# Kernel optimization log

Measured on AMD Instinct MI355X. Metric: run time of the kernel, lower is better.

## Reference

```python
import jax, jax.numpy as jnp
import numpy as np

NB_POOLS = 256


def setup_inputs() -> dict:
    key = jax.random.key(0)
    x = jax.random.normal(key, (32, 32, 32, 512), dtype=jnp.float32)
    return {"x": x}


def reference(x) -> jnp.ndarray:
    B, R, C, F = x.shape
    nb_maps = R * C
    x3 = x.reshape(B, nb_maps, F)
    # self-correlation: (B, nb_maps, nb_maps), normalized by feature count
    corr = jnp.einsum('bmf,bnf->bmn', x3, x3) / F
    corr = corr.reshape(B, R, C, nb_maps)
    # percentile ranks into the descending-sorted correlation values
    ranks = jnp.round(jnp.linspace(1.0, nb_maps - 1, NB_POOLS)).astype(jnp.int32)
    # full descending sort along last axis (matches tf.nn.top_k k=nb_maps)
    x_sort = -jnp.sort(-corr, axis=-1)
    x_pool = x_sort[..., ranks]  # (B, R, C, NB_POOLS)
    return x_pool
```

## Files before the change

### kernel.cpp

```cpp
#include <hip/hip_runtime.h>


#define NMAPS 1024
#define FDIM 512
#define TM 16
#define NT 256

typedef __attribute__((ext_vector_type(8))) short short8_t;
typedef __attribute__((ext_vector_type(4))) float f32x4;
typedef _Float16 h2 __attribute__((ext_vector_type(2)));

#define SELD 0x03020504u
#define SELA 0x07060100u

__device__ __forceinline__ h2 h2min(h2 a, h2 b) { return __builtin_elementwise_min(a, b); }
__device__ __forceinline__ h2 h2max(h2 a, h2 b) { return __builtin_elementwise_max(a, b); }

__device__ __forceinline__ unsigned h2u(h2 x) { union { h2 h; unsigned u; } t; t.h = x; return t.u; }
__device__ __forceinline__ h2 u2h(unsigned x) { union { h2 h; unsigned u; } t; t.u = x; return t.h; }

__device__ __forceinline__ h2 h2swap(h2 v) {
  unsigned u = h2u(v);
  return u2h((u >> 16) | (u << 16));
}

__device__ __forceinline__ h2 h2shfl_xor(h2 v, int m) {
  union { h2 h; int i; } u;
  u.h = v;
  u.i = __shfl_xor(u.i, m, 64);
  return u.h;
}

__device__ __forceinline__ void ce_pair(h2& a, h2& b, bool d) {
  h2 mn = h2min(a, b), mx = h2max(a, b);
  a = d ? mx : mn;
  b = d ? mn : mx;
}

__device__ __forceinline__ h2 ce1(h2 w, unsigned sel) {
  h2 s = h2swap(w);
  h2 mn = h2min(w, s), mx = h2max(w, s);
#if __has_builtin(__builtin_amdgcn_perm)
  return u2h(__builtin_amdgcn_perm(h2u(mx), h2u(mn), sel));
#else
  h2 rd; rd[0] = mx[0]; rd[1] = mn[1];
  h2 ra; ra[0] = mn[0]; ra[1] = mx[1];
  return (sel == SELD) ? rd : ra;
#endif
}

__device__ __forceinline__ void intra_merge16(h2 w[8], bool d, unsigned sel) {
  ce_pair(w[0], w[4], d); ce_pair(w[1], w[5], d); ce_pair(w[2], w[6], d); ce_pair(w[3], w[7], d);
  ce_pair(w[0], w[2], d); ce_pair(w[1], w[3], d); ce_pair(w[4], w[6], d); ce_pair(w[5], w[7], d);
  ce_pair(w[0], w[1], d); ce_pair(w[2], w[3], d); ce_pair(w[4], w[5], d); ce_pair(w[6], w[7], d);
#pragma unroll
  for (int u = 0; u < 8; ++u) w[u] = ce1(w[u], sel);
}

__device__ __forceinline__ void sort16(h2 w[8], bool d, unsigned sd, unsigned si) {
  w[0] = ce1(w[0], sd); w[1] = ce1(w[1], si); w[2] = ce1(w[2], sd); w[3] = ce1(w[3], si);
  w[4] = ce1(w[4], sd); w[5] = ce1(w[5], si); w[6] = ce1(w[6], sd); w[7] = ce1(w[7], si);
  ce_pair(w[0], w[1], d); ce_pair(w[2], w[3], !d); ce_pair(w[4], w[5], d); ce_pair(w[6], w[7], !d);
  w[0] = ce1(w[0], sd); w[1] = ce1(w[1], sd); w[2] = ce1(w[2], si); w[3] = ce1(w[3], si);
  w[4] = ce1(w[4], sd); w[5] = ce1(w[5], sd); w[6] = ce1(w[6], si); w[7] = ce1(w[7], si);
  ce_pair(w[0], w[2], d); ce_pair(w[1], w[3], d); ce_pair(w[4], w[6], !d); ce_pair(w[5], w[7], !d);
  ce_pair(w[0], w[1], d); ce_pair(w[2], w[3], d); ce_pair(w[4], w[5], !d); ce_pair(w[6], w[7], !d);
  w[0] = ce1(w[0], sd); w[1] = ce1(w[1], sd); w[2] = ce1(w[2], sd); w[3] = ce1(w[3], sd);
  w[4] = ce1(w[4], si); w[5] = ce1(w[5], si); w[6] = ce1(w[6], si); w[7] = ce1(w[7], si);
  intra_merge16(w, d, sd);
}

__device__ __forceinline__ void cross_ce(h2 w[8], int m, bool keepmax) {
#pragma unroll
  for (int u = 0; u < 8; ++u) {
    h2 p = h2shfl_xor(w[u], m);
    h2 mn = h2min(w[u], p), mx = h2max(w[u], p);
    w[u] = keepmax ? mx : mn;
  }
}

template<int K>
__device__ __forceinline__ void bitonic_stage(h2 w8[8], int lane) {
  const bool laneDesc = (K >= 16) ? ((lane & (K >> 4)) == 0) : true;
#pragma unroll
  for (int j = 512; j >= 16; j >>= 1) {
    if (j > (K >> 1)) continue;
    const int m = j >> 4;
    const bool keepmax = (((lane & m) == 0) == laneDesc);
#pragma unroll
    for (int u = 0; u < 8; ++u) {
      h2 p = h2shfl_xor(w8[u], m);
      h2 mn = h2min(w8[u], p), mx = h2max(w8[u], p);
      w8[u] = keepmax ? mx : mn;
    }
  }
#pragma unroll
  for (int j = 8; j >= 2; j >>= 1) {
    if (j > (K >> 1)) continue;
    const int jw = j >> 1;
#pragma unroll
    for (int u = 0; u < 8; ++u) {
      if ((u & jw) == 0) {
        const int v = u | jw;
        const bool desc = (K <= 8) ? (((2 * u) & K) == 0) : laneDesc;
        h2 mn = h2min(w8[u], w8[v]), mx = h2max(w8[u], w8[v]);
        w8[u] = desc ? mx : mn;
        w8[v] = desc ? mn : mx;
      }
    }
  }
#pragma unroll
  for (int u = 0; u < 8; ++u) {
    const bool desc = (K <= 8) ? (((2 * u) & K) == 0) : laneDesc;
    h2 s = h2swap(w8[u]);
    h2 mn = h2min(w8[u], s), mx = h2max(w8[u], s);
    h2 rd = (h2){mx[0], mn[1]};
    h2 ra = (h2){mn[0], mx[1]};
    w8[u] = desc ? rd : ra;
  }
}

template<int K>
__device__ __forceinline__ void bitonic_stage_tail(h2 w8[8], int lane) {
  const bool laneDesc = ((lane & (K >> 4)) == 0);
#pragma unroll
  for (int j = 512; j >= 16; j >>= 1) {
    if (j > (K >> 1)) continue;
    const int m = j >> 4;
    cross_ce(w8, m, ((lane & m) == 0) == laneDesc);
  }
  intra_merge16(w8, laneDesc, laneDesc ? SELD : SELA);
}

__device__ __forceinline__ void run_bitonic(h2 w8[8], int lane) {
  bitonic_stage<2>(w8, lane);
  bitonic_stage<4>(w8, lane);
  bitonic_stage<8>(w8, lane);
  bitonic_stage<16>(w8, lane);
  bitonic_stage<32>(w8, lane);
  bitonic_stage<64>(w8, lane);
  bitonic_stage<128>(w8, lane);
  bitonic_stage<256>(w8, lane);
  bitonic_stage<512>(w8, lane);
  bitonic_stage<1024>(w8, lane);
}

__global__ __launch_bounds__(256) void cvt_bf16_kernel(const float* __restrict__ x,
                                                       short* __restrict__ xw, int n8) {
  int i = blockIdx.x * 256 + threadIdx.x;
  if (i >= n8) return;
  const float4* x4 = reinterpret_cast<const float4*>(x);
  float4 a = x4[i * 2], c = x4[i * 2 + 1];
  float f[8] = {a.x, a.y, a.z, a.w, c.x, c.y, c.z, c.w};
  union { short8_t v; short s[8]; } o;
#pragma unroll
  for (int j = 0; j < 8; ++j) {
    unsigned u = __float_as_uint(f[j]);
    u += 0x7fffu + ((u >> 16) & 1u);
    o.s[j] = (short)(u >> 16);
  }
  reinterpret_cast<short8_t*>(xw)[i] = o.v;
}

__global__ __launch_bounds__(NT) void corr_gemm_tiled(const short* __restrict__ xw,
                                                      unsigned* __restrict__ corrW) {
  __shared__ short Asm[2][128 * 32];
  __shared__ short Bsm[2][128 * 32];
  const int tid = threadIdx.x;
  const int b = blockIdx.y;
  const int it = blockIdx.x >> 3, jt = blockIdx.x & 7;
  const int i0 = it * 128, j0 = jt * 128;
  const int lane = tid & 63;
  const int wid = tid >> 6;
  const int lr = lane & 15;
  const int kg = lane >> 4;
  const int wr = wid >> 1, wc = wid & 1;
  const short* Xb = xw + (size_t)b * NMAPS * FDIM;

  const int idxs[2] = {tid, tid + 256};
  int srcOff[2];
#pragma unroll
  for (int rp = 0; rp < 2; ++rp) {
    const int r = idxs[rp] >> 2;
    const int s = (idxs[rp] & 3) ^ ((r >> 1) & 3);
    srcOff[rp] = r * FDIM + s * 8;
  }

  f32x4 acc[4][4];
#pragma unroll
  for (int fm = 0; fm < 4; ++fm)
#pragma unroll
    for (int fn = 0; fn < 4; ++fn) acc[fm][fn] = (f32x4){0.f, 0.f, 0.f, 0.f};

#define STAGE(buf, kt)                                                                 \
  {                                                                                    \
    _Pragma("unroll") for (int rp = 0; rp < 2; ++rp) {                                 \
      const short* gA = Xb + (size_t)i0 * FDIM + srcOff[rp] + (kt) * 32;               \
      const short* gB = Xb + (size_t)j0 * FDIM + srcOff[rp] + (kt) * 32;               \
      __builtin_amdgcn_global_load_lds(                                                \
          (const __attribute__((address_space(1))) unsigned*)gA,                       \
          (__attribute__((address_space(3))) unsigned*)(Asm[buf] + idxs[rp] * 8), 16,  \
          0, 0);                                                                       \
      __builtin_amdgcn_global_load_lds(                                                \
          (const __attribute__((address_space(1))) unsigned*)gB,                       \
          (__attribute__((address_space(3))) unsigned*)(Bsm[buf] + idxs[rp] * 8), 16,  \
          0, 0);                                                                       \
    }                                                                                  \
  }

  int aOff[4], bOff[4];
#pragma unroll
  for (int f = 0; f < 4; ++f) {
    const int ra = wr * 64 + f * 16 + lr;
    const int rb = wc * 64 + f * 16 + lr;
    aOff[f] = ra * 32 + (kg ^ ((ra >> 1) & 3)) * 8;
    bOff[f] = rb * 32 + (kg ^ ((rb >> 1) & 3)) * 8;
  }

  STAGE(0, 0);
  __syncthreads();

  for (int kt = 0; kt < 16; ++kt) {
    const int cur = kt & 1;
    if (kt < 15) STAGE(cur ^ 1, kt + 1);

    short8_t a[4], bf[4];
#pragma unroll
    for (int fm = 0; fm < 4; ++fm)
      a[fm] = *reinterpret_cast<const short8_t*>(Asm[cur] + aOff[fm]);
#pragma unroll
    for (int fn = 0; fn < 4; ++fn)
      bf[fn] = *reinterpret_cast<const short8_t*>(Bsm[cur] + bOff[fn]);
#pragma unroll
    for (int fm = 0; fm < 4; ++fm)
#pragma unroll
      for (int fn = 0; fn < 4; ++fn)
        acc[fm][fn] = __builtin_amdgcn_mfma_f32_16x16x32_bf16(bf[fn], a[fm], acc[fm][fn], 0, 0, 0);

    __syncthreads();
  }
#undef STAGE

  const bool D0 = (wc == 0);
  const bool d16 = ((kg & 1) == 0) ? D0 : !D0;
  const unsigned sd16 = d16 ? SELD : SELA, si16 = d16 ? SELA : SELD;
  const bool d32 = ((kg & 2) == 0) ? D0 : !D0;

#pragma unroll
  for (int fm = 0; fm < 4; ++fm) {
    h2 w[8];
#pragma unroll
    for (int fn = 0; fn < 4; ++fn) {
      w[2 * fn] = (h2){(_Float16)acc[fm][fn][0], (_Float16)acc[fm][fn][1]};
      w[2 * fn + 1] = (h2){(_Float16)acc[fm][fn][2], (_Float16)acc[fm][fn][3]};
    }
    sort16(w, d16, sd16, si16);
    cross_ce(w, 16, ((kg & 1) == 0) == d32);
    intra_merge16(w, d32, d32 ? SELD : SELA);
    cross_ce(w, 32, ((kg & 2) == 0) == D0);
    cross_ce(w, 16, ((kg & 1) == 0) == D0);
    intra_merge16(w, D0, D0 ? SELD : SELA);
    const size_t roww = ((size_t)b * NMAPS + i0 + wr * 64 + fm * 16 + lr) * 512;
    const int wq = (j0 >> 1) + wc * 32 + kg * 8;
    union { h2 h[4]; uint4 u; } s0, s1;
    s0.h[0] = w[0]; s0.h[1] = w[1]; s0.h[2] = w[2]; s0.h[3] = w[3];
    s1.h[0] = w[4]; s1.h[1] = w[5]; s1.h[2] = w[6]; s1.h[3] = w[7];
    *reinterpret_cast<uint4*>(corrW + roww + wq) = s0.u;
    *reinterpret_cast<uint4*>(corrW + roww + wq + 4) = s1.u;
  }
}

__global__ __launch_bounds__(256) void sort_rows_kernel(const unsigned* __restrict__ corrW,
                                                        float* __restrict__ out) {
  const int tid = threadIdx.x;
  const int lane = tid & 63;
  const int row = blockIdx.x * 4 + (tid >> 6);
  const uint4* r4 = reinterpret_cast<const uint4*>(corrW + (size_t)row * 512);

  h2 w8[8];
  {
    union { uint4 u; h2 h[4]; } a, c;
    a.u = r4[lane * 2];
    c.u = r4[lane * 2 + 1];
    w8[0] = a.h[0]; w8[1] = a.h[1]; w8[2] = a.h[2]; w8[3] = a.h[3];
    w8[4] = c.h[0]; w8[5] = c.h[1]; w8[6] = c.h[2]; w8[7] = c.h[3];
  }

  bitonic_stage_tail<128>(w8, lane);
  bitonic_stage_tail<256>(w8, lane);
  bitonic_stage_tail<512>(w8, lane);
  bitonic_stage_tail<1024>(w8, lane);

  float* orow = out + (size_t)row * 256;
#pragma unroll
  for (int u = 0; u < 8; ++u) {
#pragma unroll
    for (int hh = 0; hh < 2; ++hh) {
      const int i = lane * 16 + 2 * u + hh;
      const int p = (int)rint((double)(i - 1) * (255.0 / 1022.0));
      const int rk = (int)rint(1.0 + (double)p * (1022.0 / 255.0));
      if (rk == i) orow[p] = (float)w8[u][hh] * (1.f / FDIM);
    }
  }
}

__global__ __launch_bounds__(NT) void selfcorr_mfma_kernel(const short* __restrict__ xw,
                                                           float* __restrict__ out) {
  __shared__ alignas(16) h2 SH[TM * 512];
  const int tid = threadIdx.x;
  const int b = blockIdx.y;
  const int m0 = blockIdx.x * TM;
  const int lane = tid & 63;
  const int wid = tid >> 6;
  const int lr = lane & 15;
  const int kg = lane >> 4;
  const int wc = wid * 256;
  const short* Xb = xw + (size_t)b * NMAPS * FDIM;

  f32x4 acc[16];
#pragma unroll
  for (int t = 0; t < 16; ++t) acc[t] = (f32x4){0.f, 0.f, 0.f, 0.f};

  for (int kk = 0; kk < 16; ++kk) {
    const short8_t* base = reinterpret_cast<const short8_t*>(Xb + kk * 32 + kg * 8);
    short8_t afrag = base[(size_t)(m0 + lr) * 64];
    short8_t bfrag[16];
#pragma unroll
    for (int t = 0; t < 16; ++t) bfrag[t] = base[(size_t)(wc + t * 16 + lr) * 64];
#pragma unroll
    for (int t = 0; t < 16; ++t)
      acc[t] = __builtin_amdgcn_mfma_f32_16x16x32_bf16(bfrag[t], afrag, acc[t], 0, 0, 0);
  }

  {
    const int xorv = (lr & 7) << 2;
#pragma unroll
    for (int t = 0; t < 16; ++t) {
      h2 lo = (h2){(_Float16)(acc[t][0] * (1.f / FDIM)), (_Float16)(acc[t][1] * (1.f / FDIM))};
      h2 hi = (h2){(_Float16)(acc[t][2] * (1.f / FDIM)), (_Float16)(acc[t][3] * (1.f / FDIM))};
      const int W = (wc >> 1) + t * 8 + kg * 2;
      const int phys = lr * 512 + (W ^ xorv);
      union { h2 h[2]; uint2 u; } pk;
      pk.h[0] = lo; pk.h[1] = hi;
      *reinterpret_cast<uint2*>(&SH[phys]) = pk.u;
    }
  }
  __syncthreads();

  const int rowbase = wid * 4;
  for (int rr = rowbase; rr < rowbase + 4; ++rr) {
    const int rx = (rr & 7) << 2;
    h2 w8[8];
#pragma unroll
    for (int q = 0; q < 2; ++q) {
      const int p4 = rr * 512 + ((lane * 8 + q * 4) ^ rx);
      union { uint4 u; h2 h[4]; } un;
      un.u = *reinterpret_cast<const uint4*>(&SH[p4]);
      w8[q * 4 + 0] = un.h[0]; w8[q * 4 + 1] = un.h[1];
      w8[q * 4 + 2] = un.h[2]; w8[q * 4 + 3] = un.h[3];
    }
    run_bitonic(w8, lane);
#pragma unroll
    for (int q = 0; q < 2; ++q) {
      const int p4 = rr * 512 + ((lane * 8 + q * 4) ^ rx);
      union { uint4 u; h2 h[4]; } un;
      un.h[0] = w8[q * 4 + 0]; un.h[1] = w8[q * 4 + 1];
      un.h[2] = w8[q * 4 + 2]; un.h[3] = w8[q * 4 + 3];
      *reinterpret_cast<uint4*>(&SH[p4]) = un.u;
    }
  }
  __builtin_amdgcn_wave_barrier();

#pragma unroll
  for (int i = 0; i < 16; ++i) {
    const int rr = rowbase + (i >> 2);
    const int p = lane + ((i & 3) << 6);
    const int rank = (int)rint(1.0 + (double)p * (1022.0 / 255.0));
    const int Wr = (rank >> 1) ^ ((rr & 7) << 2);
    h2 hv = SH[rr * 512 + Wr];
    out[((size_t)(b * NMAPS + m0 + rr) << 8) + p] = (float)hv[rank & 1];
  }
}

__device__ __forceinline__ int sw4(int row, int c4) {
  return (row << 8) | (c4 ^ ((c4 >> 3) & 7));
}
__device__ __forceinline__ void ce(float& a, float& b, bool desc) {
  float mn = fminf(a, b);
  float mx = fmaxf(a, b);
  a = desc ? mx : mn;
  b = desc ? mn : mx;
}

__global__ __launch_bounds__(NT) void selfcorr_pool_kernel(const float* __restrict__ x,
                                                           float* __restrict__ out) {
  __shared__ float lds[TM * NMAPS];
  float4* S4 = reinterpret_cast<float4*>(lds);
  const int tid = threadIdx.x;
  const int b = blockIdx.y;
  const int m0 = blockIdx.x * TM;
  const float4* Xb = reinterpret_cast<const float4*>(x) + (size_t)b * NMAPS * (FDIM / 4);

  float4* A4 = reinterpret_cast<float4*>(lds);
#pragma unroll
  for (int idx = tid; idx < TM * (FDIM / 4); idx += NT) {
    A4[idx] = Xb[(m0 + (idx >> 7)) * 128 + (idx & 127)];
  }
  __syncthreads();

  float acc[TM][4];
#pragma unroll
  for (int m = 0; m < TM; ++m)
#pragma unroll
    for (int j = 0; j < 4; ++j) acc[m][j] = 0.0f;

  float4 nb0 = Xb[(tid + 0) * 128];
  float4 nb1 = Xb[(tid + 256) * 128];
  float4 nb2 = Xb[(tid + 512) * 128];
  float4 nb3 = Xb[(tid + 768) * 128];
  for (int k4 = 0; k4 < 128; ++k4) {
    float4 b0 = nb0, b1 = nb1, b2 = nb2, b3 = nb3;
    const int kn = (k4 < 127) ? (k4 + 1) : 127;
    nb0 = Xb[(tid + 0) * 128 + kn];
    nb1 = Xb[(tid + 256) * 128 + kn];
    nb2 = Xb[(tid + 512) * 128 + kn];
    nb3 = Xb[(tid + 768) * 128 + kn];
#pragma unroll
    for (int m = 0; m < TM; ++m) {
      float4 a = A4[m * 128 + k4];
      acc[m][0] += a.x * b0.x + a.y * b0.y + a.z * b0.z + a.w * b0.w;
      acc[m][1] += a.x * b1.x + a.y * b1.y + a.z * b1.z + a.w * b1.w;
      acc[m][2] += a.x * b2.x + a.y * b2.y + a.z * b2.z + a.w * b2.w;
      acc[m][3] += a.x * b3.x + a.y * b3.y + a.z * b3.z + a.w * b3.w;
    }
  }
  __syncthreads();

#pragma unroll
  for (int m = 0; m < TM; ++m) {
#pragma unroll
    for (int j = 0; j < 4; ++j) {
      const int n = tid + (j << 8);
      lds[sw4(m, n >> 2) * 4 + (n & 3)] = acc[m][j] * (1.0f / FDIM);
    }
  }
  __syncthreads();

#pragma unroll
  for (int c = 0; c < 2; ++c) {
    const int cid = tid + (c << 8);
    const int row = cid >> 5;
    const int chunk = cid & 31;
    float r[32];
#pragma unroll
    for (int q = 0; q < 8; ++q) {
      float4 t = S4[sw4(row, (chunk << 3) + q)];
      r[q * 4 + 0] = t.x; r[q * 4 + 1] = t.y; r[q * 4 + 2] = t.z; r[q * 4 + 3] = t.w;
    }
    const bool D = ((chunk & 1) == 0);
#pragma unroll
    for (int k2 = 2; k2 <= 32; k2 <<= 1) {
#pragma unroll
      for (int j = k2 >> 1; j > 0; j >>= 1) {
#pragma unroll
        for (int i = 0; i < 32; ++i) {
          if ((i & j) == 0) ce(r[i], r[i | j], ((i & k2) == 0) ? D : !D);
        }
      }
    }
#pragma unroll
    for (int q = 0; q < 8; ++q) {
      S4[sw4(row, (chunk << 3) + q)] =
          make_float4(r[q * 4 + 0], r[q * 4 + 1], r[q * 4 + 2], r[q * 4 + 3]);
    }
  }
  __syncthreads();

  for (int k = 64; k <= NMAPS; k <<= 1) {
    for (int j = k >> 1; j >= 32; j >>= 1) {
      const int j4 = j >> 2;
      const int kq = k >> 2;
#pragma unroll
      for (int q = 0; q < 8; ++q) {
        const int g = tid + (q << 8);
        const int row = g >> 7;
        const int v = g & 127;
        const int i4 = ((v & ~(j4 - 1)) << 1) | (v & (j4 - 1));
        const bool desc = ((i4 & kq) == 0);
        const int ia = sw4(row, i4);
        const int ib = sw4(row, i4 + j4);
        float4 va = S4[ia];
        float4 vb = S4[ib];
        float4 lo, hi;
        lo.x = fminf(va.x, vb.x); hi.x = fmaxf(va.x, vb.x);
        lo.y = fminf(va.y, vb.y); hi.y = fmaxf(va.y, vb.y);
        lo.z = fminf(va.z, vb.z); hi.z = fmaxf(va.z, vb.z);
        lo.w = fminf(va.w, vb.w); hi.w = fmaxf(va.w, vb.w);
        S4[ia] = desc ? hi : lo;
        S4[ib] = desc ? lo : hi;
      }
      __syncthreads();
    }
#pragma unroll
    for (int c = 0; c < 2; ++c) {
      const int cid = tid + (c << 8);
      const int row = cid >> 5;
      const int chunk = cid & 31;
      const bool D = (((chunk << 5) & k) == 0);
      float r[32];
#pragma unroll
      for (int q = 0; q < 8; ++q) {
        float4 t = S4[sw4(row, (chunk << 3) + q)];
        r[q * 4 + 0] = t.x; r[q * 4 + 1] = t.y; r[q * 4 + 2] = t.z; r[q * 4 + 3] = t.w;
      }
#pragma unroll
      for (int j = 16; j > 0; j >>= 1) {
#pragma unroll
        for (int i = 0; i < 32; ++i) {
          if ((i & j) == 0) ce(r[i], r[i | j], D);
        }
      }
#pragma unroll
      for (int q = 0; q < 8; ++q) {
        S4[sw4(row, (chunk << 3) + q)] =
            make_float4(r[q * 4 + 0], r[q * 4 + 1], r[q * 4 + 2], r[q * 4 + 3]);
      }
    }
    __syncthreads();
  }

  const int p = tid;
  const int rank = (int)rint(1.0 + (double)p * (1022.0 / 255.0));
#pragma unroll
  for (int m = 0; m < TM; ++m) {
    out[((size_t)(b * NMAPS + m0 + m) << 8) + p] = lds[sw4(m, rank >> 2) * 4 + (rank & 3)];
  }
}

extern "C" void kernel_launch(void* const* d_in, const int* in_sizes, int n_in,
                              void* d_out, int out_size, void* d_ws, size_t ws_size,
                              hipStream_t stream) {
  const float* x = reinterpret_cast<const float*>(d_in[0]);
  float* out = reinterpret_cast<float*>(d_out);
  const int nelem = in_sizes[0];
  const int B = nelem / (NMAPS * FDIM);
  const size_t need_split = (size_t)nelem * 2 + (size_t)B * NMAPS * NMAPS * 2;
  if (ws_size >= need_split) {
    short* xw = reinterpret_cast<short*>(d_ws);
    unsigned* corrW = reinterpret_cast<unsigned*>((char*)d_ws + (size_t)nelem * 2);
    const int n8 = nelem / 8;
    hipLaunchKernelGGL(cvt_bf16_kernel, dim3((n8 + 255) / 256), dim3(256), 0, stream, x, xw, n8);
    hipLaunchKernelGGL(corr_gemm_tiled, dim3(64, B), dim3(NT), 0, stream, xw, corrW);
    hipLaunchKernelGGL(sort_rows_kernel, dim3(B * NMAPS / 4), dim3(256), 0, stream, corrW, out);
  } else if (ws_size >= (size_t)nelem * 2) {
    short* xw = reinterpret_cast<short*>(d_ws);
    const int n8 = nelem / 8;
    hipLaunchKernelGGL(cvt_bf16_kernel, dim3((n8 + 255) / 256), dim3(256), 0, stream, x, xw, n8);
    hipLaunchKernelGGL(selfcorr_mfma_kernel, dim3(NMAPS / TM, B), dim3(NT), 0, stream, xw, out);
  } else {
    hipLaunchKernelGGL(selfcorr_pool_kernel, dim3(NMAPS / TM, B), dim3(NT), 0, stream, x, out);
  }
}
```

Before: 167.8 us.

## Use 8-wave GEMM blocks with full 128-column sorted segments in epilogue

The correlation GEMM block grows from 4 to 8 waves. Each wave now owns one 16-row strip across all 128 columns (8 MFMA accumulators) instead of a 64x64 quadrant. The epilogue sorts the whole 128-wide row segment per lane group via new 32-element register merges, so the row-sort kernel can drop its first bitonic stage. This shifts sorting work into the GEMM epilogue and raises per-block parallelism, but each wave reloads its A fragment against all B fragments and holds more registers per thread.

```diff
diff --git a/kernel.cpp b/kernel.cpp
--- a/kernel.cpp
+++ b/kernel.cpp
@@ -70,13 +70,34 @@
   intra_merge16(w, d, sd);
 }
 
-__device__ __forceinline__ void cross_ce(h2 w[8], int m, bool keepmax) {
-#pragma unroll
-  for (int u = 0; u < 8; ++u) {
+__device__ __forceinline__ void merge32(h2 w[16], bool d) {
+  const unsigned sel = d ? SELD : SELA;
+#pragma unroll
+  for (int u = 0; u < 8; ++u) ce_pair(w[u], w[u + 8], d);
+#pragma unroll
+  for (int u = 0; u < 16; ++u)
+    if ((u & 4) == 0) ce_pair(w[u], w[u | 4], d);
+#pragma unroll
+  for (int u = 0; u < 16; ++u)
+    if ((u & 2) == 0) ce_pair(w[u], w[u | 2], d);
+#pragma unroll
+  for (int u = 0; u < 16; ++u)
+    if ((u & 1) == 0) ce_pair(w[u], w[u | 1], d);
+#pragma unroll
+  for (int u = 0; u < 16; ++u) w[u] = ce1(w[u], sel);
+}
+
+template<int N>
+__device__ __forceinline__ void cross_ceN(h2* w, int m, bool keepmax) {
+#pragma unroll
+  for (int u = 0; u < N; ++u) {
     h2 p = h2shfl_xor(w[u], m);
     h2 mn = h2min(w[u], p), mx = h2max(w[u], p);
     w[u] = keepmax ? mx : mn;
   }
+}
+__device__ __forceinline__ void cross_ce(h2 w[8], int m, bool keepmax) {
+  cross_ceN<8>(w, m, keepmax);
 }
 
 template<int K>
@@ -162,8 +183,8 @@
   reinterpret_cast<short8_t*>(xw)[i] = o.v;
 }
 
-__global__ __launch_bounds__(NT) void corr_gemm_tiled(const short* __restrict__ xw,
-                                                      unsigned* __restrict__ corrW) {
+__global__ __launch_bounds__(512) void corr_gemm_tiled(const short* __restrict__ xw,
+                                                       unsigned* __restrict__ corrW) {
   __shared__ short Asm[2][128 * 32];
   __shared__ short Bsm[2][128 * 32];
   const int tid = threadIdx.x;
@@ -171,50 +192,39 @@
   const int it = blockIdx.x >> 3, jt = blockIdx.x & 7;
   const int i0 = it * 128, j0 = jt * 128;
   const int lane = tid & 63;
-  const int wid = tid >> 6;
+  const int w = tid >> 6;
   const int lr = lane & 15;
   const int kg = lane >> 4;
-  const int wr = wid >> 1, wc = wid & 1;
   const short* Xb = xw + (size_t)b * NMAPS * FDIM;
 
-  const int idxs[2] = {tid, tid + 256};
-  int srcOff[2];
-#pragma unroll
-  for (int rp = 0; rp < 2; ++rp) {
-    const int r = idxs[rp] >> 2;
-    const int s = (idxs[rp] & 3) ^ ((r >> 1) & 3);
-    srcOff[rp] = r * FDIM + s * 8;
-  }
-
-  f32x4 acc[4][4];
-#pragma unroll
-  for (int fm = 0; fm < 4; ++fm)
-#pragma unroll
-    for (int fn = 0; fn < 4; ++fn) acc[fm][fn] = (f32x4){0.f, 0.f, 0.f, 0.f};
-
-#define STAGE(buf, kt)                                                                 \
-  {                                                                                    \
-    _Pragma("unroll") for (int rp = 0; rp < 2; ++rp) {                                 \
-      const short* gA = Xb + (size_t)i0 * FDIM + srcOff[rp] + (kt) * 32;               \
-      const short* gB = Xb + (size_t)j0 * FDIM + srcOff[rp] + (kt) * 32;               \
-      __builtin_amdgcn_global_load_lds(                                                \
-          (const __attribute__((address_space(1))) unsigned*)gA,                       \
-          (__attribute__((address_space(3))) unsigned*)(Asm[buf] + idxs[rp] * 8), 16,  \
-          0, 0);                                                                       \
-      __builtin_amdgcn_global_load_lds(                                                \
-          (const __attribute__((address_space(1))) unsigned*)gB,                       \
-          (__attribute__((address_space(3))) unsigned*)(Bsm[buf] + idxs[rp] * 8), 16,  \
-          0, 0);                                                                       \
-    }                                                                                  \
-  }
-
-  int aOff[4], bOff[4];
-#pragma unroll
-  for (int f = 0; f < 4; ++f) {
-    const int ra = wr * 64 + f * 16 + lr;
-    const int rb = wc * 64 + f * 16 + lr;
-    aOff[f] = ra * 32 + (kg ^ ((ra >> 1) & 3)) * 8;
-    bOff[f] = rb * 32 + (kg ^ ((rb >> 1) & 3)) * 8;
+  const int sr = tid >> 2;
+  const int ss = (tid & 3) ^ ((sr >> 1) & 3);
+  const int srcOff = sr * FDIM + ss * 8;
+  const int dstOff = tid * 8;
+
+  const int rowa = w * 16 + lr;
+  const int aOff = rowa * 32 + (kg ^ ((rowa >> 1) & 3)) * 8;
+  int bOff[8];
+#pragma unroll
+  for (int fn = 0; fn < 8; ++fn) {
+    const int rowb = fn * 16 + lr;
+    bOff[fn] = rowb * 32 + (kg ^ ((rowb >> 1) & 3)) * 8;
+  }
+
+  f32x4 acc[8];
+#pragma unroll
+  for (int fn = 0; fn < 8; ++fn) acc[fn] = (f32x4){0.f, 0.f, 0.f, 0.f};
+
+#define STAGE(buf, kt)                                                                \
+  {                                                                                   \
+    const short* gA = Xb + (size_t)i0 * FDIM + srcOff + (kt) * 32;                    \
+    const short* gB = Xb + (size_t)j0 * FDIM + srcOff + (kt) * 32;                    \
+    __builtin_amdgcn_global_load_lds(                                                 \
+        (const __attribute__((address_space(1))) unsigned*)gA,                        \
+        (__attribute__((address_space(3))) unsigned*)(Asm[buf] + dstOff), 16, 0, 0);  \
+    __builtin_amdgcn_global_load_lds(                                                 \
+        (const __attribute__((address_space(1))) unsigned*)gB,                        \
+        (__attribute__((address_space(3))) unsigned*)(Bsm[buf] + dstOff), 16, 0, 0);  \
   }
 
   STAGE(0, 0);
@@ -224,49 +234,46 @@
     const int cur = kt & 1;
     if (kt < 15) STAGE(cur ^ 1, kt + 1);
 
-    short8_t a[4], bf[4];
-#pragma unroll
-    for (int fm = 0; fm < 4; ++fm)
-      a[fm] = *reinterpret_cast<const short8_t*>(Asm[cur] + aOff[fm]);
-#pragma unroll
-    for (int fn = 0; fn < 4; ++fn)
+    short8_t a = *reinterpret_cast<const short8_t*>(Asm[cur] + aOff);
+    short8_t bf[8];
+#pragma unroll
+    for (int fn = 0; fn < 8; ++fn)
       bf[fn] = *reinterpret_cast<const short8_t*>(Bsm[cur] + bOff[fn]);
 #pragma unroll
-    for (int fm = 0; fm < 4; ++fm)
-#pragma unroll
-      for (int fn = 0; fn < 4; ++fn)
-        acc[fm][fn] = __builtin_amdgcn_mfma_f32_16x16x32_bf16(bf[fn], a[fm], acc[fm][fn], 0, 0, 0);
+    for (int fn = 0; fn < 8; ++fn)
+      acc[fn] = __builtin_amdgcn_mfma_f32_16x16x32_bf16(bf[fn], a, acc[fn], 0, 0, 0);
 
     __syncthreads();
   }
 #undef STAGE
 
-  const bool D0 = (wc == 0);
-  const bool d16 = ((kg & 1) == 0) ? D0 : !D0;
-  const unsigned sd16 = d16 ? SELD : SELA, si16 = d16 ? SELA : SELD;
-  const bool d32 = ((kg & 2) == 0) ? D0 : !D0;
-
-#pragma unroll
-  for (int fm = 0; fm < 4; ++fm) {
-    h2 w[8];
-#pragma unroll
-    for (int fn = 0; fn < 4; ++fn) {
-      w[2 * fn] = (h2){(_Float16)acc[fm][fn][0], (_Float16)acc[fm][fn][1]};
-      w[2 * fn + 1] = (h2){(_Float16)acc[fm][fn][2], (_Float16)acc[fm][fn][3]};
-    }
-    sort16(w, d16, sd16, si16);
-    cross_ce(w, 16, ((kg & 1) == 0) == d32);
-    intra_merge16(w, d32, d32 ? SELD : SELA);
-    cross_ce(w, 32, ((kg & 2) == 0) == D0);
-    cross_ce(w, 16, ((kg & 1) == 0) == D0);
-    intra_merge16(w, D0, D0 ? SELD : SELA);
-    const size_t roww = ((size_t)b * NMAPS + i0 + wr * 64 + fm * 16 + lr) * 512;
-    const int wq = (j0 >> 1) + wc * 32 + kg * 8;
-    union { h2 h[4]; uint4 u; } s0, s1;
-    s0.h[0] = w[0]; s0.h[1] = w[1]; s0.h[2] = w[2]; s0.h[3] = w[3];
-    s1.h[0] = w[4]; s1.h[1] = w[5]; s1.h[2] = w[6]; s1.h[3] = w[7];
+  {
+    const bool D128 = ((jt & 1) == 0);
+    const bool d64 = ((kg & 2) == 0);
+    const bool d32 = ((kg & 1) == 0);
+    h2 W[16];
+#pragma unroll
+    for (int fn = 0; fn < 8; ++fn) {
+      W[2 * fn] = (h2){(_Float16)acc[fn][0], (_Float16)acc[fn][1]};
+      W[2 * fn + 1] = (h2){(_Float16)acc[fn][2], (_Float16)acc[fn][3]};
+    }
+    sort16(W, true, SELD, SELA);
+    sort16(W + 8, false, SELA, SELD);
+    merge32(W, d32);
+    cross_ceN<16>(W, 16, d32 == d64);
+    merge32(W, d64);
+    cross_ceN<16>(W, 32, d64 == D128);
+    cross_ceN<16>(W, 16, d32 == D128);
+    merge32(W, D128);
+    const size_t roww = ((size_t)b * NMAPS + i0 + w * 16 + lr) * 512;
+    const int wq = (j0 >> 1) + kg * 16;
+    union { h2 h[4]; uint4 u; } s0, s1, s2, s3;
+#pragma unroll
+    for (int q = 0; q < 4; ++q) { s0.h[q] = W[q]; s1.h[q] = W[4 + q]; s2.h[q] = W[8 + q]; s3.h[q] = W[12 + q]; }
     *reinterpret_cast<uint4*>(corrW + roww + wq) = s0.u;
     *reinterpret_cast<uint4*>(corrW + roww + wq + 4) = s1.u;
+    *reinterpret_cast<uint4*>(corrW + roww + wq + 8) = s2.u;
+    *reinterpret_cast<uint4*>(corrW + roww + wq + 12) = s3.u;
   }
 }
 
@@ -286,7 +293,6 @@
     w8[4] = c.h[0]; w8[5] = c.h[1]; w8[6] = c.h[2]; w8[7] = c.h[3];
   }
 
-  bitonic_stage_tail<128>(w8, lane);
   bitonic_stage_tail<256>(w8, lane);
   bitonic_stage_tail<512>(w8, lane);
   bitonic_stage_tail<1024>(w8, lane);
@@ -550,7 +556,7 @@
     unsigned* corrW = reinterpret_cast<unsigned*>((char*)d_ws + (size_t)nelem * 2);
     const int n8 = nelem / 8;
     hipLaunchKernelGGL(cvt_bf16_kernel, dim3((n8 + 255) / 256), dim3(256), 0, stream, x, xw, n8);
-    hipLaunchKernelGGL(corr_gemm_tiled, dim3(64, B), dim3(NT), 0, stream, xw, corrW);
+    hipLaunchKernelGGL(corr_gemm_tiled, dim3(64, B), dim3(512), 0, stream, xw, corrW);
     hipLaunchKernelGGL(sort_rows_kernel, dim3(B * NMAPS / 4), dim3(256), 0, stream, corrW, out);
   } else if (ws_size >= (size_t)nelem * 2) {
     short* xw = reinterpret_cast<short*>(d_ws);
```

Measured after the change: 164.0 us. 2.3% less time.
